# Kernel optimization log

Hardware: AMD Instinct MI355X
Metric: run time of the kernel (lower is better)

The kernel has to match this reference:

```python
import jax, jax.numpy as jnp
import numpy as np

DIM = 4096
N_HEADS = 32
N_KV_HEADS = 8
HEAD_DIM = DIM // N_HEADS  # 128
N_REP = N_HEADS // N_KV_HEADS  # 4
BSZ_LIST = (16, 16)
START_POS_LIST = (2048, 1024)
SEQLEN = 1
CACHE_LEN = 2080
ROPE_THETA = 500000.0


def setup_inputs() -> dict:
    key = jax.random.key(0)
    ks = jax.random.split(key, 10)
    total_bsz = sum(BSZ_LIST)
    x = jax.random.normal(ks[0], (total_bsz, SEQLEN, DIM), dtype=jnp.float32)
    scale = 0.02
    wq = jax.random.normal(ks[1], (DIM, DIM), dtype=jnp.float32) * scale
    wk = jax.random.normal(ks[2], (N_KV_HEADS * HEAD_DIM, DIM), dtype=jnp.float32) * scale
    wv = jax.random.normal(ks[3], (N_KV_HEADS * HEAD_DIM, DIM), dtype=jnp.float32) * scale
    wo = jax.random.normal(ks[4], (DIM, DIM), dtype=jnp.float32) * scale
    cache_k0 = jax.random.normal(ks[5], (BSZ_LIST[0], CACHE_LEN, N_KV_HEADS, HEAD_DIM), dtype=jnp.float32)
    cache_v0 = jax.random.normal(ks[6], (BSZ_LIST[0], CACHE_LEN, N_KV_HEADS, HEAD_DIM), dtype=jnp.float32)
    cache_k1 = jax.random.normal(ks[7], (BSZ_LIST[1], CACHE_LEN, N_KV_HEADS, HEAD_DIM), dtype=jnp.float32)
    cache_v1 = jax.random.normal(ks[8], (BSZ_LIST[1], CACHE_LEN, N_KV_HEADS, HEAD_DIM), dtype=jnp.float32)
    # real RoPE tables (cos/sin of the complex freqs_cis)
    inv_freq = 1.0 / (ROPE_THETA ** (np.arange(0, HEAD_DIM, 2, dtype=np.float32) / HEAD_DIM))
    t = np.arange(CACHE_LEN, dtype=np.float32)
    ang = np.outer(t, inv_freq)  # [CACHE_LEN, HEAD_DIM/2]
    freqs_cos = jnp.asarray(np.cos(ang), dtype=jnp.float32)
    freqs_sin = jnp.asarray(np.sin(ang), dtype=jnp.float32)
    return {"x": x, "wq": wq, "wk": wk, "wv": wv, "wo": wo,
            "cache_k0": cache_k0, "cache_v0": cache_v0,
            "cache_k1": cache_k1, "cache_v1": cache_v1,
            "freqs_cos": freqs_cos, "freqs_sin": freqs_sin}


def _rope(v, cos, sin):
    # v: [b, s, h, d]; cos/sin: [s, d/2] -> interleaved complex rotation
    vr = v.reshape(v.shape[:-1] + (HEAD_DIM // 2, 2))
    a, b = vr[..., 0], vr[..., 1]
    c = cos[None, :, None, :]
    s = sin[None, :, None, :]
    out = jnp.stack([a * c - b * s, a * s + b * c], axis=-1)
    return out.reshape(v.shape)


def _group_attention(xq, xk, xv, cache_k, cache_v, start_pos, freqs_cos, freqs_sin):
    bsz, seqlen = xq.shape[0], xq.shape[1]
    cos = freqs_cos[start_pos:start_pos + seqlen]
    sin = freqs_sin[start_pos:start_pos + seqlen]
    xq = _rope(xq, cos, sin)
    xk = _rope(xk, cos, sin)
    # functional equivalent of cache[:, start_pos:start_pos+seqlen] = new; read [:start_pos+seqlen]
    keys = jnp.concatenate([cache_k[:, :start_pos], xk], axis=1)    # [b, kv, kvh, d]
    values = jnp.concatenate([cache_v[:, :start_pos], xv], axis=1)
    keys = jnp.repeat(keys, N_REP, axis=2)      # GQA repeat -> [b, kv, h, d]
    values = jnp.repeat(values, N_REP, axis=2)
    scores = jnp.einsum('bqhd,bkhd->bhqk', xq, keys) / jnp.sqrt(jnp.float32(HEAD_DIM))
    if seqlen > 1:
        kv_len = start_pos + seqlen
        q_pos = jnp.arange(seqlen)[:, None] + start_pos
        k_pos = jnp.arange(kv_len)[None, :]
        scores = jnp.where(k_pos <= q_pos, scores, jnp.float32(-jnp.inf))
    probs = jax.nn.softmax(scores.astype(jnp.float32), axis=-1).astype(xq.dtype)
    out = jnp.einsum('bhqk,bkhd->bqhd', probs, values)
    return out.reshape(bsz, seqlen, -1)


def reference(x, wq, wk, wv, wo, cache_k0, cache_v0, cache_k1, cache_v1, freqs_cos, freqs_sin):
    total_bsz, seqlen, _ = x.shape
    xq_ = x @ wq.T
    xk_ = x @ wk.T
    xv_ = x @ wv.T
    caches = ((cache_k0, cache_v0), (cache_k1, cache_v1))
    outputs = []
    start = 0
    for i, bsz in enumerate(BSZ_LIST):
        xq = xq_[start:start + bsz].reshape(bsz, seqlen, N_HEADS, HEAD_DIM)
        xk = xk_[start:start + bsz].reshape(bsz, seqlen, N_KV_HEADS, HEAD_DIM)
        xv = xv_[start:start + bsz].reshape(bsz, seqlen, N_KV_HEADS, HEAD_DIM)
        start += bsz
        ck, cv = caches[i]
        outputs.append(_group_attention(xq, xk, xv, ck, cv, START_POS_LIST[i], freqs_cos, freqs_sin))
    output = jnp.concatenate(outputs, axis=0)  # [total_bsz, seqlen, dim]
    return output @ wo.T
```

## Files before the change

### kernel.cpp

```cpp
#include <hip/hip_runtime.h>
#include <hip/hip_bf16.h>

#define DIM       4096
#define NHEADS    32
#define NKV       8
#define HD        128
#define NREP      4
#define CACHELEN  2080
#define QKVN      6144
#define BSZ       32
#define SP0       2048
#define SP1       1024
#define KCHUNK    512
#define NSPLK     8
#define SPLITROWS 256
#define MAXSPL    8
#define PSTRIDE   132

typedef unsigned short u16;
typedef unsigned int   u32;
typedef __bf16 bf16x8 __attribute__((ext_vector_type(8)));
typedef float  f32x4  __attribute__((ext_vector_type(4)));

#define LD8(dst, p) do { \
    *(float4*)(dst)       = *(const float4*)(p); \
    *(float4*)((dst) + 4) = *(const float4*)((p) + 4); } while (0)

static __device__ __forceinline__ bf16x8 pack8(float4 lo, float4 hi) {
    bf16x8 r;
    r[0] = (__bf16)lo.x; r[1] = (__bf16)lo.y; r[2] = (__bf16)lo.z; r[3] = (__bf16)lo.w;
    r[4] = (__bf16)hi.x; r[5] = (__bf16)hi.y; r[6] = (__bf16)hi.z; r[7] = (__bf16)hi.w;
    return r;
}

__global__ __launch_bounds__(256) void qkv_gemm(
    const float* __restrict__ x, const float* __restrict__ wq,
    const float* __restrict__ wk, const float* __restrict__ wv,
    float* __restrict__ qkv_part)
{
    const int lane = threadIdx.x & 63;
    const int w    = threadIdx.x >> 6;
    const int n0   = (blockIdx.x * 4 + w) * 16;
    const float* W; int nr;
    if (n0 < 4096)      { W = wq; nr = n0; }
    else if (n0 < 5120) { W = wk; nr = n0 - 4096; }
    else                { W = wv; nr = n0 - 5120; }
    const int c16  = lane & 15;
    const int quad = lane >> 4;
    const int k0   = blockIdx.y * KCHUNK;
    const float* ap0 = x + (size_t)c16 * DIM + k0 + quad * 8;
    const float* ap1 = ap0 + 16 * DIM;
    const float* bp  = W + (size_t)(nr + c16) * DIM + k0 + quad * 8;
    f32x4 acc0 = {0.f,0.f,0.f,0.f}, acc1 = {0.f,0.f,0.f,0.f};
#pragma unroll 4
    for (int kk = 0; kk < KCHUNK; kk += 32) {
        bf16x8 a0 = pack8(*(const float4*)(ap0 + kk), *(const float4*)(ap0 + kk + 4));
        bf16x8 a1 = pack8(*(const float4*)(ap1 + kk), *(const float4*)(ap1 + kk + 4));
        bf16x8 b  = pack8(*(const float4*)(bp  + kk), *(const float4*)(bp  + kk + 4));
        acc0 = __builtin_amdgcn_mfma_f32_16x16x32_bf16(a0, b, acc0, 0, 0, 0);
        acc1 = __builtin_amdgcn_mfma_f32_16x16x32_bf16(a1, b, acc1, 0, 0, 0);
    }
    float* dst = qkv_part + (size_t)blockIdx.y * (BSZ * QKVN);
#pragma unroll
    for (int r = 0; r < 4; ++r) {
        int m = quad * 4 + r;
        dst[(size_t)m * QKVN + n0 + c16]        = acc0[r];
        dst[(size_t)(m + 16) * QKVN + n0 + c16] = acc1[r];
    }
}

__global__ __launch_bounds__(256) void sum_splits(
    const float4* __restrict__ in, float4* __restrict__ out, int n4)
{
    int i = blockIdx.x * 256 + threadIdx.x;
    if (i >= n4) return;
    float4 s0 = in[i];
#pragma unroll
    for (int s = 1; s < NSPLK; ++s) {
        float4 t = in[(size_t)s * n4 + i];
        s0.x += t.x; s0.y += t.y; s0.z += t.z; s0.w += t.w;
    }
    out[i] = s0;
}

__global__ __launch_bounds__(256) void attn_decode_split(
    const float* __restrict__ qkv,
    const float* __restrict__ ck0, const float* __restrict__ cv0,
    const float* __restrict__ ck1, const float* __restrict__ cv1,
    const float* __restrict__ fcos, const float* __restrict__ fsin,
    float* __restrict__ part)
{
    const int tid  = threadIdx.x;
    const int lane = tid & 63;
    const int w    = tid >> 6;
    const int quad = lane >> 4;
    const int ch   = lane & 15;
    const int db   = ch * 8;

    int b, g, s, sp;
    const float *CK, *CV;
    if ((int)blockIdx.x < 1024) {
        int bid = blockIdx.x;
        b = bid >> 6; g = (bid >> 3) & 7; s = bid & 7; sp = SP0;
        size_t off = (size_t)b * CACHELEN * NKV * HD;
        CK = ck0 + off; CV = cv0 + off;
    } else {
        int bid = blockIdx.x - 1024;
        b = 16 + (bid >> 5); g = (bid >> 2) & 7; s = bid & 3; sp = SP1;
        size_t off = (size_t)(b - 16) * CACHELEN * NKV * HD;
        CK = ck1 + off; CV = cv1 + off;
    }

    float cs[4], sn[4];
#pragma unroll
    for (int i = 0; i < 4; ++i) {
        int fi = sp * (HD / 2) + ch * 4 + i;
        cs[i] = fcos[fi];
        sn[i] = fsin[fi];
    }
    const float rs = 0.08838834764831845f;

    float qv[4][8];
#pragma unroll
    for (int h = 0; h < 4; ++h) {
        const float* qp = qkv + (size_t)b * QKVN + (g * 4 + h) * HD + db;
        float t[8];
#pragma unroll
        for (int j = 0; j < 8; ++j) t[j] = qp[j];
#pragma unroll
        for (int i = 0; i < 4; ++i) {
            float e = t[2 * i], o = t[2 * i + 1];
            qv[h][2 * i]     = (e * cs[i] - o * sn[i]) * rs;
            qv[h][2 * i + 1] = (e * sn[i] + o * cs[i]) * rs;
        }
    }

    const bool has_new = (s == 0) && (w == 0);
    float kn[8], vn[8];
    if (has_new) {
        const float* kp = qkv + (size_t)b * QKVN + 4096 + g * HD + db;
        const float* vp = qkv + (size_t)b * QKVN + 5120 + g * HD + db;
        float t[8];
#pragma unroll
        for (int j = 0; j < 8; ++j) t[j] = kp[j];
#pragma unroll
        for (int i = 0; i < 4; ++i) {
            float e = t[2 * i], o = t[2 * i + 1];
            kn[2 * i]     = e * cs[i] - o * sn[i];
            kn[2 * i + 1] = e * sn[i] + o * cs[i];
        }
#pragma unroll
        for (int j = 0; j < 8; ++j) vn[j] = vp[j];
    }

    float m_[4] = {-INFINITY, -INFINITY, -INFINITY, -INFINITY};
    float l_[4] = {0.f, 0.f, 0.f, 0.f};
    float acc[4][8];
#pragma unroll
    for (int h = 0; h < 4; ++h)
#pragma unroll
        for (int j = 0; j < 8; ++j) acc[h][j] = 0.f;

    const size_t rstride = NKV * HD;
    const float* kp0 = CK + g * HD + db + (size_t)(s * SPLITROWS + w * 8 + quad) * rstride;
    const float* vp0 = CV + g * HD + db + (size_t)(s * SPLITROWS + w * 8 + quad) * rstride;

    auto do_batch = [&](const float* kpB, const float* vpB, bool fold_new) {
        float Ka[4][2][8];
#pragma unroll
        for (int it = 0; it < 4; ++it) {
            const float* kq = kpB + (size_t)(it * 32) * rstride;
            LD8(Ka[it][0], kq);
            LD8(Ka[it][1], kq + 4 * rstride);
        }
        float d[4][2][4];
#pragma unroll
        for (int it = 0; it < 4; ++it)
#pragma unroll
            for (int r = 0; r < 2; ++r)
#pragma unroll
                for (int h = 0; h < 4; ++h) d[it][r][h] = 0.f;
#pragma unroll
        for (int it = 0; it < 4; ++it)
#pragma unroll
            for (int j = 0; j < 8; ++j)
#pragma unroll
                for (int h = 0; h < 4; ++h) {
                    d[it][0][h] = fmaf(qv[h][j], Ka[it][0][j], d[it][0][h]);
                    d[it][1][h] = fmaf(qv[h][j], Ka[it][1][j], d[it][1][h]);
                }
#pragma unroll
        for (int off = 1; off < 16; off <<= 1)
#pragma unroll
            for (int it = 0; it < 4; ++it)
#pragma unroll
                for (int r = 0; r < 2; ++r)
#pragma unroll
                    for (int h = 0; h < 4; ++h)
                        d[it][r][h] += __shfl_xor(d[it][r][h], off);
        float bm[4];
#pragma unroll
        for (int h = 0; h < 4; ++h) {
            float a0 = fmaxf(fmaxf(d[0][0][h], d[0][1][h]), fmaxf(d[1][0][h], d[1][1][h]));
            float a1 = fmaxf(fmaxf(d[2][0][h], d[2][1][h]), fmaxf(d[3][0][h], d[3][1][h]));
            bm[h] = fmaxf(a0, a1);
        }
#pragma unroll
        for (int off = 16; off <= 32; off <<= 1)
#pragma unroll
            for (int h = 0; h < 4; ++h)
                bm[h] = fmaxf(bm[h], __shfl_xor(bm[h], off));
        float dn[4] = {0.f, 0.f, 0.f, 0.f};
        if (fold_new) {
#pragma unroll
            for (int j = 0; j < 8; ++j)
#pragma unroll
                for (int h = 0; h < 4; ++h) dn[h] = fmaf(qv[h][j], kn[j], dn[h]);
#pragma unroll
            for (int off = 1; off < 16; off <<= 1)
#pragma unroll
                for (int h = 0; h < 4; ++h) dn[h] += __shfl_xor(dn[h], off);
#pragma unroll
            for (int h = 0; h < 4; ++h) bm[h] = fmaxf(bm[h], dn[h]);
        }
        float Va[4][2][8];
#pragma unroll
        for (int it = 0; it < 4; ++it) {
            const float* vq = vpB + (size_t)(it * 32) * rstride;
            LD8(Va[it][0], vq);
            LD8(Va[it][1], vq + 4 * rstride);
        }
#pragma unroll
        for (int h = 0; h < 4; ++h) {
            float mn = fmaxf(m_[h], bm[h]);
            float sl = __expf(m_[h] - mn);
            float lb = 0.f;
#pragma unroll
            for (int it = 0; it < 4; ++it)
#pragma unroll
                for (int r = 0; r < 2; ++r) {
                    float p = __expf(d[it][r][h] - mn);
                    d[it][r][h] = p;
                    lb += p;
                }
            l_[h] = l_[h] * sl + lb;
#pragma unroll
            for (int j = 0; j < 8; ++j) {
                float a = acc[h][j] * sl;
#pragma unroll
                for (int it = 0; it < 4; ++it) {
                    a = fmaf(d[it][0][h], Va[it][0][j], a);
                    a = fmaf(d[it][1][h], Va[it][1][j], a);
                }
                acc[h][j] = a;
            }
            m_[h] = mn;
            if (fold_new && quad == 0) {
                float pn = __expf(dn[h] - mn);
                l_[h] += pn;
#pragma unroll
                for (int j = 0; j < 8; ++j) acc[h][j] = fmaf(pn, vn[j], acc[h][j]);
            }
        }
    };

    do_batch(kp0, vp0, false);
    do_batch(kp0 + 128 * rstride, vp0 + 128 * rstride, has_new);

#pragma unroll
    for (int off = 16; off <= 32; off <<= 1) {
#pragma unroll
        for (int h = 0; h < 4; ++h) {
            l_[h] += __shfl_xor(l_[h], off);
#pragma unroll
            for (int j = 0; j < 8; ++j) acc[h][j] += __shfl_xor(acc[h][j], off);
        }
    }

    __shared__ float ls_m[4][4];
    __shared__ float ls_l[4][4];
    __shared__ float ls_a[4][4][16][8];
    if (lane == 0) {
#pragma unroll
        for (int h = 0; h < 4; ++h) { ls_m[w][h] = m_[h]; ls_l[w][h] = l_[h]; }
    }
    if (quad == 0) {
#pragma unroll
        for (int h = 0; h < 4; ++h)
#pragma unroll
            for (int j = 0; j < 8; ++j) ls_a[w][h][ch][j] = acc[h][j];
    }
    __syncthreads();
    if (tid < 64) {
        int h = tid >> 4, c = tid & 15;
        float mm = -INFINITY, ll = 0.f, ac[8] = {0.f,0.f,0.f,0.f,0.f,0.f,0.f,0.f};
#pragma unroll
        for (int w2 = 0; w2 < 4; ++w2) {
            float m2 = ls_m[w2][h], l2 = ls_l[w2][h];
            float mn = fmaxf(mm, m2);
            float s1 = __expf(mm - mn), s2 = __expf(m2 - mn);
            ll = ll * s1 + l2 * s2;
#pragma unroll
            for (int j = 0; j < 8; ++j) ac[j] = ac[j] * s1 + ls_a[w2][h][c][j] * s2;
            mm = mn;
        }
        int bg = b * 8 + g;
        float* pp = part + ((((size_t)bg * MAXSPL + s) * 4 + h) * PSTRIDE);
        float4 o0, o1;
        o0.x = ac[0]; o0.y = ac[1]; o0.z = ac[2]; o0.w = ac[3];
        o1.x = ac[4]; o1.y = ac[5]; o1.z = ac[6]; o1.w = ac[7];
        *(float4*)(pp + c * 8)     = o0;
        *(float4*)(pp + c * 8 + 4) = o1;
        if (c == 0) { pp[128] = mm; pp[129] = ll; }
    }
}

__global__ __launch_bounds__(64) void attn_reduce(
    const float* __restrict__ part, float* __restrict__ attn)
{
    const int lane = threadIdx.x;
    const int h = lane >> 4, c = lane & 15;
    const int bg = blockIdx.x;
    const int b = bg >> 3, g = bg & 7;
    const int nspl = (b < 16) ? (SP0 / SPLITROWS) : (SP1 / SPLITROWS);
    const float* pb = part + (size_t)bg * MAXSPL * 4 * PSTRIDE;

    float mm = -INFINITY, ll = 0.f, ac[8] = {0.f,0.f,0.f,0.f,0.f,0.f,0.f,0.f};
    for (int s = 0; s < nspl; ++s) {
        const float* pp = pb + ((size_t)s * 4 + h) * PSTRIDE;
        float m2 = pp[128], l2 = pp[129];
        float4 a0 = *(const float4*)(pp + c * 8);
        float4 a1 = *(const float4*)(pp + c * 8 + 4);
        float a2[8] = {a0.x, a0.y, a0.z, a0.w, a1.x, a1.y, a1.z, a1.w};
        float mn = fmaxf(mm, m2);
        float s1 = __expf(mm - mn), s2 = __expf(m2 - mn);
        ll = ll * s1 + l2 * s2;
#pragma unroll
        for (int j = 0; j < 8; ++j) ac[j] = ac[j] * s1 + a2[j] * s2;
        mm = mn;
    }
    float inv = 1.f / ll;
    float* op = attn + (size_t)b * DIM + (g * 4 + h) * HD + c * 8;
    float4 o0, o1;
    o0.x = ac[0] * inv; o0.y = ac[1] * inv; o0.z = ac[2] * inv; o0.w = ac[3] * inv;
    o1.x = ac[4] * inv; o1.y = ac[5] * inv; o1.z = ac[6] * inv; o1.w = ac[7] * inv;
    *(float4*)op       = o0;
    *(float4*)(op + 4) = o1;
}

__global__ __launch_bounds__(256) void out_gemm(
    const float* __restrict__ A, const float* __restrict__ wo,
    float* __restrict__ out_part)
{
    const int lane = threadIdx.x & 63;
    const int w    = threadIdx.x >> 6;
    const int n0   = (blockIdx.x * 4 + w) * 16;
    const int c16  = lane & 15;
    const int quad = lane >> 4;
    const int k0   = blockIdx.y * KCHUNK;
    const float* ap0 = A + (size_t)c16 * DIM + k0 + quad * 8;
    const float* ap1 = ap0 + 16 * DIM;
    const float* bp  = wo + (size_t)(n0 + c16) * DIM + k0 + quad * 8;
    f32x4 acc0 = {0.f,0.f,0.f,0.f}, acc1 = {0.f,0.f,0.f,0.f};
#pragma unroll 4
    for (int kk = 0; kk < KCHUNK; kk += 32) {
        bf16x8 a0 = pack8(*(const float4*)(ap0 + kk), *(const float4*)(ap0 + kk + 4));
        bf16x8 a1 = pack8(*(const float4*)(ap1 + kk), *(const float4*)(ap1 + kk + 4));
        bf16x8 b  = pack8(*(const float4*)(bp  + kk), *(const float4*)(bp  + kk + 4));
        acc0 = __builtin_amdgcn_mfma_f32_16x16x32_bf16(a0, b, acc0, 0, 0, 0);
        acc1 = __builtin_amdgcn_mfma_f32_16x16x32_bf16(a1, b, acc1, 0, 0, 0);
    }
    float* dst = out_part + (size_t)blockIdx.y * (BSZ * DIM);
#pragma unroll
    for (int r = 0; r < 4; ++r) {
        int m = quad * 4 + r;
        dst[(size_t)m * DIM + n0 + c16]        = acc0[r];
        dst[(size_t)(m + 16) * DIM + n0 + c16] = acc1[r];
    }
}

extern "C" void kernel_launch(void* const* d_in, const int* in_sizes, int n_in,
                              void* d_out, int out_size, void* d_ws, size_t ws_size,
                              hipStream_t stream)
{
    const float* x   = (const float*)d_in[0];
    const float* wq  = (const float*)d_in[1];
    const float* wk  = (const float*)d_in[2];
    const float* wv  = (const float*)d_in[3];
    const float* wo  = (const float*)d_in[4];
    const float* ck0 = (const float*)d_in[5];
    const float* cv0 = (const float*)d_in[6];
    const float* ck1 = (const float*)d_in[7];
    const float* cv1 = (const float*)d_in[8];
    const float* fc  = (const float*)d_in[9];
    const float* fs  = (const float*)d_in[10];

    float* W = (float*)d_ws;
    float* gparts  = W;
    float* qkv     = gparts + (size_t)NSPLK * BSZ * QKVN;
    float* part    = qkv + BSZ * QKVN;
    float* attn    = part + (size_t)BSZ * NKV * MAXSPL * 4 * PSTRIDE;
    float* out     = (float*)d_out;

    qkv_gemm<<<dim3(QKVN / 64, NSPLK), 256, 0, stream>>>(x, wq, wk, wv, gparts);
    sum_splits<<<dim3(BSZ * QKVN / 1024), 256, 0, stream>>>((const float4*)gparts, (float4*)qkv, BSZ * QKVN / 4);
    attn_decode_split<<<dim3(1024 + 512), 256, 0, stream>>>(qkv, ck0, cv0, ck1, cv1, fc, fs, part);
    attn_reduce<<<dim3(BSZ * NKV), 64, 0, stream>>>(part, attn);
    out_gemm<<<dim3(DIM / 64, NSPLK), 256, 0, stream>>>(attn, wo, gparts);
    sum_splits<<<dim3(BSZ * DIM / 1024), 256, 0, stream>>>((const float4*)gparts, (float4*)out, BSZ * DIM / 4);
}
```

Baseline: 571.7 us.

## Fuse QKV split-K reduction into attention and double attention KV splits

Removes the sum_splits kernel after the QKV GEMM: the attention kernel now sums the eight split-K partials itself when it loads q, k and v. The KV cache is cut into twice as many splits (128 rows each, up to 16 per group). Each attention block therefore handles one batch of rows, and the online-softmax rescaling between batches is dropped. Both GEMM loops are unrolled 8 instead of 4, and the output reduction uses 64-thread blocks. The aim is to save a launch and a round trip through global memory for q/k/v, and to put more blocks to work streaming the bandwidth-bound KV cache. The cost is redundant partial-sum loads across blocks and more partial results for attn_reduce to combine.

Measured after the change: 622.7 us. 1.09x slower.

```diff
diff --git a/kernel.cpp b/kernel.cpp
--- a/kernel.cpp
+++ b/kernel.cpp
@@ -13,8 +13,10 @@
 #define SP1       1024
 #define KCHUNK    512
 #define NSPLK     8
-#define SPLITROWS 256
-#define MAXSPL    8
+#define QSLICE    (BSZ * QKVN)
+#define OSLICE    (BSZ * DIM)
+#define SPLITROWS 128
+#define MAXSPL    16
 #define PSTRIDE   132
 
 typedef unsigned short u16;
@@ -31,6 +33,20 @@
     r[0] = (__bf16)lo.x; r[1] = (__bf16)lo.y; r[2] = (__bf16)lo.z; r[3] = (__bf16)lo.w;
     r[4] = (__bf16)hi.x; r[5] = (__bf16)hi.y; r[6] = (__bf16)hi.z; r[7] = (__bf16)hi.w;
     return r;
+}
+
+static __device__ __forceinline__ void ld8_sum(float* dst, const float* p) {
+    float4 lo = *(const float4*)p;
+    float4 hi = *(const float4*)(p + 4);
+#pragma unroll
+    for (int sl = 1; sl < NSPLK; ++sl) {
+        float4 a = *(const float4*)(p + (size_t)sl * QSLICE);
+        float4 b = *(const float4*)(p + (size_t)sl * QSLICE + 4);
+        lo.x += a.x; lo.y += a.y; lo.z += a.z; lo.w += a.w;
+        hi.x += b.x; hi.y += b.y; hi.z += b.z; hi.w += b.w;
+    }
+    dst[0] = lo.x; dst[1] = lo.y; dst[2] = lo.z; dst[3] = lo.w;
+    dst[4] = hi.x; dst[5] = hi.y; dst[6] = hi.z; dst[7] = hi.w;
 }
 
 __global__ __launch_bounds__(256) void qkv_gemm(
@@ -52,7 +68,7 @@
     const float* ap1 = ap0 + 16 * DIM;
     const float* bp  = W + (size_t)(nr + c16) * DIM + k0 + quad * 8;
     f32x4 acc0 = {0.f,0.f,0.f,0.f}, acc1 = {0.f,0.f,0.f,0.f};
-#pragma unroll 4
+#pragma unroll 8
     for (int kk = 0; kk < KCHUNK; kk += 32) {
         bf16x8 a0 = pack8(*(const float4*)(ap0 + kk), *(const float4*)(ap0 + kk + 4));
         bf16x8 a1 = pack8(*(const float4*)(ap1 + kk), *(const float4*)(ap1 + kk + 4));
@@ -60,7 +76,7 @@
         acc0 = __builtin_amdgcn_mfma_f32_16x16x32_bf16(a0, b, acc0, 0, 0, 0);
         acc1 = __builtin_amdgcn_mfma_f32_16x16x32_bf16(a1, b, acc1, 0, 0, 0);
     }
-    float* dst = qkv_part + (size_t)blockIdx.y * (BSZ * QKVN);
+    float* dst = qkv_part + (size_t)blockIdx.y * QSLICE;
 #pragma unroll
     for (int r = 0; r < 4; ++r) {
         int m = quad * 4 + r;
@@ -69,22 +85,8 @@
     }
 }
 
-__global__ __launch_bounds__(256) void sum_splits(
-    const float4* __restrict__ in, float4* __restrict__ out, int n4)
-{
-    int i = blockIdx.x * 256 + threadIdx.x;
-    if (i >= n4) return;
-    float4 s0 = in[i];
-#pragma unroll
-    for (int s = 1; s < NSPLK; ++s) {
-        float4 t = in[(size_t)s * n4 + i];
-        s0.x += t.x; s0.y += t.y; s0.z += t.z; s0.w += t.w;
-    }
-    out[i] = s0;
-}
-
 __global__ __launch_bounds__(256) void attn_decode_split(
-    const float* __restrict__ qkv,
+    const float* __restrict__ qkv_part,
     const float* __restrict__ ck0, const float* __restrict__ cv0,
     const float* __restrict__ ck1, const float* __restrict__ cv1,
     const float* __restrict__ fcos, const float* __restrict__ fsin,
@@ -99,14 +101,14 @@
 
     int b, g, s, sp;
     const float *CK, *CV;
-    if ((int)blockIdx.x < 1024) {
+    if ((int)blockIdx.x < 2048) {
         int bid = blockIdx.x;
-        b = bid >> 6; g = (bid >> 3) & 7; s = bid & 7; sp = SP0;
+        b = bid >> 7; g = (bid >> 4) & 7; s = bid & 15; sp = SP0;
         size_t off = (size_t)b * CACHELEN * NKV * HD;
         CK = ck0 + off; CV = cv0 + off;
     } else {
-        int bid = blockIdx.x - 1024;
-        b = 16 + (bid >> 5); g = (bid >> 2) & 7; s = bid & 3; sp = SP1;
+        int bid = blockIdx.x - 2048;
+        b = 16 + (bid >> 6); g = (bid >> 3) & 7; s = bid & 7; sp = SP1;
         size_t off = (size_t)(b - 16) * CACHELEN * NKV * HD;
         CK = ck1 + off; CV = cv1 + off;
     }
@@ -123,10 +125,8 @@
     float qv[4][8];
 #pragma unroll
     for (int h = 0; h < 4; ++h) {
-        const float* qp = qkv + (size_t)b * QKVN + (g * 4 + h) * HD + db;
         float t[8];
-#pragma unroll
-        for (int j = 0; j < 8; ++j) t[j] = qp[j];
+        ld8_sum(t, qkv_part + (size_t)b * QKVN + (g * 4 + h) * HD + db);
 #pragma unroll
         for (int i = 0; i < 4; ++i) {
             float e = t[2 * i], o = t[2 * i + 1];
@@ -138,22 +138,18 @@
     const bool has_new = (s == 0) && (w == 0);
     float kn[8], vn[8];
     if (has_new) {
-        const float* kp = qkv + (size_t)b * QKVN + 4096 + g * HD + db;
-        const float* vp = qkv + (size_t)b * QKVN + 5120 + g * HD + db;
         float t[8];
-#pragma unroll
-        for (int j = 0; j < 8; ++j) t[j] = kp[j];
+        ld8_sum(t, qkv_part + (size_t)b * QKVN + 4096 + g * HD + db);
 #pragma unroll
         for (int i = 0; i < 4; ++i) {
             float e = t[2 * i], o = t[2 * i + 1];
             kn[2 * i]     = e * cs[i] - o * sn[i];
             kn[2 * i + 1] = e * sn[i] + o * cs[i];
         }
-#pragma unroll
-        for (int j = 0; j < 8; ++j) vn[j] = vp[j];
-    }
-
-    float m_[4] = {-INFINITY, -INFINITY, -INFINITY, -INFINITY};
+        ld8_sum(vn, qkv_part + (size_t)b * QKVN + 5120 + g * HD + db);
+    }
+
+    float m_[4];
     float l_[4] = {0.f, 0.f, 0.f, 0.f};
     float acc[4][8];
 #pragma unroll
@@ -162,10 +158,10 @@
         for (int j = 0; j < 8; ++j) acc[h][j] = 0.f;
 
     const size_t rstride = NKV * HD;
-    const float* kp0 = CK + g * HD + db + (size_t)(s * SPLITROWS + w * 8 + quad) * rstride;
-    const float* vp0 = CV + g * HD + db + (size_t)(s * SPLITROWS + w * 8 + quad) * rstride;
-
-    auto do_batch = [&](const float* kpB, const float* vpB, bool fold_new) {
+    const float* kpB = CK + g * HD + db + (size_t)(s * SPLITROWS + w * 8 + quad) * rstride;
+    const float* vpB = CV + g * HD + db + (size_t)(s * SPLITROWS + w * 8 + quad) * rstride;
+
+    {
         float Ka[4][2][8];
 #pragma unroll
         for (int it = 0; it < 4; ++it) {
@@ -211,7 +207,7 @@
             for (int h = 0; h < 4; ++h)
                 bm[h] = fmaxf(bm[h], __shfl_xor(bm[h], off));
         float dn[4] = {0.f, 0.f, 0.f, 0.f};
-        if (fold_new) {
+        if (has_new) {
 #pragma unroll
             for (int j = 0; j < 8; ++j)
 #pragma unroll
@@ -232,8 +228,7 @@
         }
 #pragma unroll
         for (int h = 0; h < 4; ++h) {
-            float mn = fmaxf(m_[h], bm[h]);
-            float sl = __expf(m_[h] - mn);
+            float mn = bm[h];
             float lb = 0.f;
 #pragma unroll
             for (int it = 0; it < 4; ++it)
@@ -243,10 +238,10 @@
                     d[it][r][h] = p;
                     lb += p;
                 }
-            l_[h] = l_[h] * sl + lb;
+            l_[h] = lb;
 #pragma unroll
             for (int j = 0; j < 8; ++j) {
-                float a = acc[h][j] * sl;
+                float a = 0.f;
 #pragma unroll
                 for (int it = 0; it < 4; ++it) {
                     a = fmaf(d[it][0][h], Va[it][0][j], a);
@@ -255,17 +250,14 @@
                 acc[h][j] = a;
             }
             m_[h] = mn;
-            if (fold_new && quad == 0) {
+            if (has_new && quad == 0) {
                 float pn = __expf(dn[h] - mn);
                 l_[h] += pn;
 #pragma unroll
                 for (int j = 0; j < 8; ++j) acc[h][j] = fmaf(pn, vn[j], acc[h][j]);
             }
         }
-    };
-
-    do_batch(kp0, vp0, false);
-    do_batch(kp0 + 128 * rstride, vp0 + 128 * rstride, has_new);
+    }
 
 #pragma unroll
     for (int off = 16; off <= 32; off <<= 1) {
@@ -362,7 +354,7 @@
     const float* ap1 = ap0 + 16 * DIM;
     const float* bp  = wo + (size_t)(n0 + c16) * DIM + k0 + quad * 8;
     f32x4 acc0 = {0.f,0.f,0.f,0.f}, acc1 = {0.f,0.f,0.f,0.f};
-#pragma unroll 4
+#pragma unroll 8
     for (int kk = 0; kk < KCHUNK; kk += 32) {
         bf16x8 a0 = pack8(*(const float4*)(ap0 + kk), *(const float4*)(ap0 + kk + 4));
         bf16x8 a1 = pack8(*(const float4*)(ap1 + kk), *(const float4*)(ap1 + kk + 4));
@@ -370,13 +362,27 @@
         acc0 = __builtin_amdgcn_mfma_f32_16x16x32_bf16(a0, b, acc0, 0, 0, 0);
         acc1 = __builtin_amdgcn_mfma_f32_16x16x32_bf16(a1, b, acc1, 0, 0, 0);
     }
-    float* dst = out_part + (size_t)blockIdx.y * (BSZ * DIM);
+    float* dst = out_part + (size_t)blockIdx.y * OSLICE;
 #pragma unroll
     for (int r = 0; r < 4; ++r) {
         int m = quad * 4 + r;
         dst[(size_t)m * DIM + n0 + c16]        = acc0[r];
         dst[(size_t)(m + 16) * DIM + n0 + c16] = acc1[r];
     }
+}
+
+__global__ __launch_bounds__(64) void out_reduce(
+    const float4* __restrict__ in, float4* __restrict__ out, int n4)
+{
+    int i = blockIdx.x * 64 + threadIdx.x;
+    if (i >= n4) return;
+    float4 s0 = in[i];
+#pragma unroll
+    for (int s = 1; s < NSPLK; ++s) {
+        float4 t = in[(size_t)s * n4 + i];
+        s0.x += t.x; s0.y += t.y; s0.z += t.z; s0.w += t.w;
+    }
+    out[i] = s0;
 }
 
 extern "C" void kernel_launch(void* const* d_in, const int* in_sizes, int n_in,
@@ -395,17 +401,14 @@
     const float* fc  = (const float*)d_in[9];
     const float* fs  = (const float*)d_in[10];
 
-    float* W = (float*)d_ws;
-    float* gparts  = W;
-    float* qkv     = gparts + (size_t)NSPLK * BSZ * QKVN;
-    float* part    = qkv + BSZ * QKVN;
+    float* gparts  = (float*)d_ws;
+    float* part    = gparts + (size_t)NSPLK * QSLICE;
     float* attn    = part + (size_t)BSZ * NKV * MAXSPL * 4 * PSTRIDE;
     float* out     = (float*)d_out;
 
     qkv_gemm<<<dim3(QKVN / 64, NSPLK), 256, 0, stream>>>(x, wq, wk, wv, gparts);
-    sum_splits<<<dim3(BSZ * QKVN / 1024), 256, 0, stream>>>((const float4*)gparts, (float4*)qkv, BSZ * QKVN / 4);
-    attn_decode_split<<<dim3(1024 + 512), 256, 0, stream>>>(qkv, ck0, cv0, ck1, cv1, fc, fs, part);
+    attn_decode_split<<<dim3(2048 + 1024), 256, 0, stream>>>(gparts, ck0, cv0, ck1, cv1, fc, fs, part);
     attn_reduce<<<dim3(BSZ * NKV), 64, 0, stream>>>(part, attn);
     out_gemm<<<dim3(DIM / 64, NSPLK), 256, 0, stream>>>(attn, wo, gparts);
-    sum_splits<<<dim3(BSZ * DIM / 1024), 256, 0, stream>>>((const float4*)gparts, (float4*)out, BSZ * DIM / 4);
-}
+    out_reduce<<<dim3(OSLICE / 4 / 64), 64, 0, stream>>>((const float4*)gparts, (float4*)out, OSLICE / 4);
+}
```
